# Optimization experiments

Hardware: AMD Instinct MI355X
Metric: run time of the kernel (lower is better)

## Reference

```python
import jax, jax.numpy as jnp
import numpy as np

S, NL = 64, 5000          # num_sequences, num_labels
PD, LD = 1024, 768        # protein / label embedding dims
DIM, OD = 512, 512        # latent_dim, output_dim


def setup_inputs() -> dict:
    key = jax.random.key(0)
    ks = jax.random.split(key, 8)
    sc = lambda f: 1.0 / np.sqrt(f).astype(np.float32)
    return {
        "P_f": jax.random.normal(ks[0], (S, PD), jnp.float32),
        "label_emb": jax.random.normal(ks[1], (NL, LD), jnp.float32),
        "W_p": jax.random.normal(ks[2], (DIM, PD), jnp.float32) * sc(PD),
        "W_l": jax.random.normal(ks[3], (DIM, LD), jnp.float32) * sc(LD),
        "W1": jax.random.normal(ks[4], (OD, 2 * DIM), jnp.float32) * sc(2 * DIM),
        "b1": jnp.zeros((OD,), jnp.float32),
        "W2": jax.random.normal(ks[5], (OD, OD), jnp.float32) * sc(OD),
        "b2": jnp.zeros((OD,), jnp.float32),
        "W3": jax.random.normal(ks[6], (1, OD), jnp.float32) * sc(OD),
        "b3": jnp.zeros((1,), jnp.float32),
        "L": jnp.arange(NL, dtype=jnp.int64),
    }


def reference(P_f, label_emb, W_p, W_l, W1, b1, W2, b2, W3, b3, L):
    # label lookup (cached_label_embeddings(L)) + linear projections
    L_f = label_emb[L]                      # [NL, LD]
    P_e = P_f @ W_p.T                       # [S, DIM]
    L_e = L_f @ W_l.T                       # [NL, DIM]
    # joint cat([P_e_expanded, L_e_expanded]) @ W1.T  ==  P-side + L-side GEMMs,
    # broadcast-summed (avoids materializing the [S*NL, 2*DIM] concat)
    hp = P_e @ W1[:, :DIM].T                # [S, OD]
    hl = L_e @ W1[:, DIM:].T                # [NL, OD]
    h = jax.nn.relu(hp[:, None, :] + hl[None, :, :] + b1)   # [S, NL, OD]
    h = jax.nn.relu(jnp.einsum("snd,od->sno", h, W2) + b2)  # [S, NL, OD]
    logits = jnp.einsum("sno,o->sn", h, W3[0]) + b3[0]      # [S, NL]
    return logits
```

## Files before the change

### kernel.cpp

```cpp
#include <hip/hip_runtime.h>
#include <hip/hip_bf16.h>

typedef short short8 __attribute__((ext_vector_type(8)));
typedef float f32x4 __attribute__((ext_vector_type(4)));

#define S_   64
#define NL_  5000
#define PD_  1024
#define LD_  768
#define DIM_ 512
#define OD_  512

#define BK     32
#define KSTEPS 16
#define NT_M   79
#define HL_RT  157

__device__ __forceinline__ ushort f2bf(float f) {
    union { float f; unsigned u; } v; v.f = f;
    unsigned r = v.u + 0x7fffu + ((v.u >> 16) & 1u);
    return (ushort)(r >> 16);
}
__device__ __forceinline__ float bf2f(ushort h) {
    union { unsigned u; float f; } v; v.u = ((unsigned)h) << 16;
    return v.f;
}
__device__ __forceinline__ int swz(int row, int kslot) {
    return (row * 64 + kslot * 16) ^ (((row >> 1) & 7) << 4);
}

__device__ __forceinline__ void proj8(
    float* Af , const float* __restrict__ A, int lda, int K,
    const float* __restrict__ W, int ldw, const float* __restrict__ bias,
    float* __restrict__ C, int o0, int t) {
    const int s = t & 63, og = t >> 6;
    const int oA = o0 + og * 2, oB = oA + 1;
    float acc0 = 0.f, acc1 = 0.f;
    for (int ck = 0; ck < K; ck += 256) {
        __syncthreads();
#pragma unroll
        for (int it = 0; it < 16; it++) {
            int r = it * 4 + (t >> 6);
            float4 v = *(const float4*)(A + (size_t)r * lda + ck + (t & 63) * 4);
            *(float4*)(Af + r * 258 + (t & 63) * 4) = v;
        }
        __syncthreads();
        const float* w0 = W + (size_t)oA * ldw + ck;
        const float* w1 = W + (size_t)oB * ldw + ck;
        const float* ar = Af + s * 258;
#pragma unroll 8
        for (int k4 = 0; k4 < 64; k4++) {
            f32x4 a4 = *(const f32x4*)(ar + k4 * 4);
            float4 v0 = *(const float4*)(w0 + k4 * 4);
            float4 v1 = *(const float4*)(w1 + k4 * 4);
            acc0 += a4[0] * v0.x + a4[1] * v0.y + a4[2] * v0.z + a4[3] * v0.w;
            acc1 += a4[0] * v1.x + a4[1] * v1.y + a4[2] * v1.z + a4[3] * v1.w;
        }
    }
    C[s * DIM_ + oA] = acc0 + (bias ? bias[oA] : 0.f);
    C[s * DIM_ + oB] = acc1 + (bias ? bias[oB] : 0.f);
}

__global__ __launch_bounds__(256) void k_pre1(
    const float* __restrict__ W2, const float* __restrict__ W_l,
    const float* __restrict__ W1, const float* __restrict__ P_f,
    const float* __restrict__ W_p,
    char* __restrict__ panel, ushort* __restrict__ MlT, float* __restrict__ P_e) {
    __shared__ float lbuf[64 * 258];
    int b = blockIdx.x, t = threadIdx.x;
    if (b < 128) {
        int c = b * 256 + t;
        int o = c >> 6, rem = c & 63, kt = rem >> 2, kslot = rem & 3;
        const float* src = W2 + o * DIM_ + kt * BK + kslot * 8;
        float4 v0 = *(const float4*)src;
        float4 v1 = *(const float4*)(src + 4);
        union { ushort u[8]; short8 v; } pk;
        pk.u[0] = f2bf(v0.x); pk.u[1] = f2bf(v0.y); pk.u[2] = f2bf(v0.z); pk.u[3] = f2bf(v0.w);
        pk.u[4] = f2bf(v1.x); pk.u[5] = f2bf(v1.y); pk.u[6] = f2bf(v1.z); pk.u[7] = f2bf(v1.w);
        *(short8*)(panel + kt * 32768 + (o >> 4) * 1024 + kslot * 256 + (o & 15) * 16) = pk.v;
    } else if (b < 320) {
        float (*w1r)[DIM_] = (float (*)[DIM_])lbuf;
        int bx = b - 128;
        int o0 = (bx / 3) * 8;
        int ld = (bx % 3) * 256 + t;
        for (int i = t; i < 8 * DIM_; i += 256)
            w1r[i >> 9][i & 511] = W1[(o0 + (i >> 9)) * (2 * DIM_) + DIM_ + (i & 511)];
        __syncthreads();
        float acc[8] = {};
        for (int dim = 0; dim < DIM_; dim++) {
            float wl = W_l[dim * LD_ + ld];
#pragma unroll
            for (int oi = 0; oi < 8; oi++) acc[oi] += w1r[oi][dim] * wl;
        }
#pragma unroll
        for (int oi = 0; oi < 8; oi++) MlT[(o0 + oi) * LD_ + ld] = f2bf(acc[oi]);
    } else {
        proj8(lbuf, P_f, PD_, PD_, W_p, PD_, nullptr, P_e, (b - 320) * 8, t);
    }
}

__global__ __launch_bounds__(256) void k_pre2(
    const float* __restrict__ P_e, const float* __restrict__ W1,
    const float* __restrict__ b1, const float* __restrict__ emb,
    const int* __restrict__ L, const ushort* __restrict__ MlT,
    float* __restrict__ hpb, ushort* __restrict__ hlB) {
    __shared__ float lbuf[64 * 258];
    int b = blockIdx.x, t = threadIdx.x;
    if (b < 64) {
        proj8(lbuf, P_e, DIM_, DIM_, W1, 2 * DIM_, b1, hpb, b * 8, t);
    } else {
        int hb = b - 64;
        int rblk = hb % HL_RT, oh = hb / HL_RT;
        int r0 = rblk * 32;
        int w = t >> 6, l = t & 63, lg = l >> 4, ll = l & 15;
        const float* arow[2];
#pragma unroll
        for (int mt = 0; mt < 2; mt++) {
            int r = r0 + mt * 16 + ll;
            if (r >= NL_) r = NL_ - 1;
            arow[mt] = emb + (size_t)L[r] * LD_ + lg * 8;
        }
        f32x4 acc[2][4] = {};
        for (int k = 0; k < LD_; k += 32) {
            short8 a[2], bf[4];
#pragma unroll
            for (int mt = 0; mt < 2; mt++) {
                float4 v0 = *(const float4*)(arow[mt] + k);
                float4 v1 = *(const float4*)(arow[mt] + k + 4);
                union { ushort u[8]; short8 v; } pk;
                pk.u[0] = f2bf(v0.x); pk.u[1] = f2bf(v0.y);
                pk.u[2] = f2bf(v0.z); pk.u[3] = f2bf(v0.w);
                pk.u[4] = f2bf(v1.x); pk.u[5] = f2bf(v1.y);
                pk.u[6] = f2bf(v1.z); pk.u[7] = f2bf(v1.w);
                a[mt] = pk.v;
            }
#pragma unroll
            for (int ot = 0; ot < 4; ot++) {
                int o = oh * 256 + w * 64 + ot * 16 + ll;
                bf[ot] = *(const short8*)(MlT + o * LD_ + k + lg * 8);
            }
#pragma unroll
            for (int mt = 0; mt < 2; mt++)
#pragma unroll
                for (int ot = 0; ot < 4; ot++)
                    acc[mt][ot] = __builtin_amdgcn_mfma_f32_16x16x32_bf16(a[mt], bf[ot], acc[mt][ot], 0, 0, 0);
        }
#pragma unroll
        for (int mt = 0; mt < 2; mt++)
#pragma unroll
            for (int ot = 0; ot < 4; ot++)
#pragma unroll
                for (int reg = 0; reg < 4; reg++) {
                    int r = r0 + mt * 16 + lg * 4 + reg;
                    if (r < NL_)
                        hlB[(size_t)r * DIM_ + oh * 256 + w * 64 + ot * 16 + ll] = f2bf(acc[mt][ot][reg]);
                }
    }
}

__global__ __launch_bounds__(512, 2) void k_main2(
    const ushort* __restrict__ hlB, const float* __restrict__ hpb,
    const char* __restrict__ panel, const float* __restrict__ b2,
    const float* __restrict__ W3, const float* __restrict__ b3,
    float* __restrict__ out) {
    __shared__ f32x4 ldsv[1024];
    char* lds = (char*)ldsv;
    const int t = threadIdx.x;
    const int n0 = blockIdx.x * 64, s0 = blockIdx.y * 2;
    const int w = t >> 6, lane = t & 63, lg = lane >> 4, ll = lane & 15;
    const int wr = w >> 2, wc = w & 3;

    const int arow = t >> 2, akslot = t & 3;
    int an = n0 + (arow & 63); if (an >= NL_) an = NL_ - 1;
    const ushort* hlsrc = hlB + (size_t)an * DIM_ + akslot * 8;
    const float*  hpsrc = hpb + (s0 + (arow >> 6)) * DIM_ + akslot * 8;
    const int awz = swz(arow, akslot);

    const int abase = swz(wr * 64 + ll, lg);
    const char* bbase = panel + (wc * 8) * 1024 + lane * 16;

    f32x4 acc[4][8] = {};

    auto packA = [&](int buf, short8 hv, float4 p0, float4 p1) {
        float hp8[8] = { p0.x, p0.y, p0.z, p0.w, p1.x, p1.y, p1.z, p1.w };
        float x[8];
#pragma unroll
        for (int e = 0; e < 8; e++) {
            float s = bf2f((ushort)hv[e]) + hp8[e];
            x[e] = s > 0.f ? s : 0.f;
        }
        union { __hip_bfloat162 h2[4]; short8 v; } pk;
#pragma unroll
        for (int e = 0; e < 4; e++)
            pk.h2[e] = __float22bfloat162_rn(make_float2(x[2 * e], x[2 * e + 1]));
        *(short8*)(lds + buf * 8192 + awz) = pk.v;
    };

    {
        short8 hv = *(const short8*)(hlsrc);
        float4 p0 = *(const float4*)(hpsrc);
        float4 p1 = *(const float4*)(hpsrc + 4);
        packA(0, hv, p0, p1);
        asm volatile("s_waitcnt lgkmcnt(0)" ::: "memory");
        __builtin_amdgcn_s_barrier();
    }
    short8 bq0[4], bq1[4];
#pragma unroll
    for (int j = 0; j < 4; j++) bq0[j] = *(const short8*)(bbase + j * 1024);

    for (int kt = 0; kt < KSTEPS; kt++) {
        const char* bkt = bbase + kt * 32768;
        short8 hv; float4 p0, p1;
        if (kt + 1 < KSTEPS) {
            hv = *(const short8*)(hlsrc + (kt + 1) * BK);
            p0 = *(const float4*)(hpsrc + (kt + 1) * BK);
            p1 = *(const float4*)(hpsrc + (kt + 1) * BK + 4);
        }
        const char* A = lds + (kt & 1) * 8192;
        short8 a[4];
#pragma unroll
        for (int mt = 0; mt < 4; mt++) a[mt] = *(const short8*)(A + abase + mt * 1024);
#pragma unroll
        for (int j = 0; j < 4; j++) bq1[j] = *(const short8*)(bkt + 4096 + j * 1024);
        __builtin_amdgcn_s_setprio(1);
#pragma unroll
        for (int mt = 0; mt < 4; mt++)
#pragma unroll
            for (int j = 0; j < 4; j++)
                acc[mt][j] = __builtin_amdgcn_mfma_f32_16x16x32_bf16(a[mt], bq0[j], acc[mt][j], 0, 0, 0);
        __builtin_amdgcn_s_setprio(0);
        if (kt + 1 < KSTEPS)
#pragma unroll
            for (int j = 0; j < 4; j++) bq0[j] = *(const short8*)(bkt + 32768 + j * 1024);
        __builtin_amdgcn_s_setprio(1);
#pragma unroll
        for (int mt = 0; mt < 4; mt++)
#pragma unroll
            for (int j = 0; j < 4; j++)
                acc[mt][4 + j] = __builtin_amdgcn_mfma_f32_16x16x32_bf16(a[mt], bq1[j], acc[mt][4 + j], 0, 0, 0);
        __builtin_amdgcn_s_setprio(0);
        if (kt + 1 < KSTEPS) packA((kt + 1) & 1, hv, p0, p1);
        asm volatile("s_waitcnt lgkmcnt(0)" ::: "memory");
        __builtin_amdgcn_s_barrier();
    }

    float* logit = (float*)lds;
    if (t < 128) logit[t] = 0.f;
    __syncthreads();
#pragma unroll
    for (int mt = 0; mt < 4; mt++) {
        float p4[4] = { 0.f, 0.f, 0.f, 0.f };
#pragma unroll
        for (int ot = 0; ot < 8; ot++) {
            int o = wc * 128 + ot * 16 + ll;
            float bb = b2[o], w3 = W3[o];
#pragma unroll
            for (int reg = 0; reg < 4; reg++) {
                float v = acc[mt][ot][reg] + bb;
                v = v > 0.f ? v : 0.f;
                p4[reg] += v * w3;
            }
        }
#pragma unroll
        for (int m = 1; m < 16; m <<= 1)
#pragma unroll
            for (int reg = 0; reg < 4; reg++) p4[reg] += __shfl_xor(p4[reg], m, 64);
        if (ll == 0)
#pragma unroll
            for (int reg = 0; reg < 4; reg++)
                atomicAdd(&logit[wr * 64 + mt * 16 + lg * 4 + reg], p4[reg]);
    }
    __syncthreads();
    if (t < 128) {
        int n = n0 + (t & 63);
        int s = s0 + (t >> 6);
        if (n < NL_) out[(size_t)s * NL_ + n] = logit[t] + b3[0];
    }
}

extern "C" void kernel_launch(void* const* d_in, const int* in_sizes, int n_in,
                              void* d_out, int out_size, void* d_ws, size_t ws_size,
                              hipStream_t stream) {
    const float* P_f = (const float*)d_in[0];
    const float* emb = (const float*)d_in[1];
    const float* W_p = (const float*)d_in[2];
    const float* W_l = (const float*)d_in[3];
    const float* W1  = (const float*)d_in[4];
    const float* b1  = (const float*)d_in[5];
    const float* W2  = (const float*)d_in[6];
    const float* b2  = (const float*)d_in[7];
    const float* W3  = (const float*)d_in[8];
    const float* b3  = (const float*)d_in[9];
    const int*   L   = (const int*)d_in[10];
    float* out = (float*)d_out;

    char* ws = (char*)d_ws;
    size_t off = 0;
    auto alloc = [&](size_t bytes) {
        void* p = ws + off;
        off = (off + bytes + 255) & ~(size_t)255;
        return p;
    };
    char*   panel = (char*)alloc((size_t)KSTEPS * 32768);
    ushort* MlT   = (ushort*)alloc((size_t)OD_ * LD_ * 2);
    float*  P_e   = (float*)alloc((size_t)S_ * DIM_ * 4);
    float*  hpb   = (float*)alloc((size_t)S_ * DIM_ * 4);
    ushort* hlB   = (ushort*)alloc((size_t)NL_ * DIM_ * 2);

    k_pre1<<<384, 256, 0, stream>>>(W2, W_l, W1, P_f, W_p, panel, MlT, P_e);
    k_pre2<<<378, 256, 0, stream>>>(P_e, W1, b1, emb, L, MlT, hpb, hlB);
    k_main2<<<dim3(NT_M, 32), 512, 0, stream>>>(hlB, hpb, panel, b2, W3, b3, out);
}
```

Measured before the change: 273.5 us.

## Give each wave a private A-tile slice to drop per-k-step barriers

Each wave now builds its own copy of the relu(hl+hp) A operand in a private LDS slice, with each lane handling one row. This removes the block-wide barrier after every k-step. The cost is redundant global loads and conversion work, since the four waves sharing a row group each rebuild the same tile. LDS use also grows fourfold to 64KB, which may reduce occupancy below 2 blocks per CU, and the loads within a step are no longer prefetched one iteration ahead.

```diff
diff --git a/kernel.cpp b/kernel.cpp
--- a/kernel.cpp
+++ b/kernel.cpp
@@ -24,9 +24,6 @@
 __device__ __forceinline__ float bf2f(ushort h) {
     union { unsigned u; float f; } v; v.u = ((unsigned)h) << 16;
     return v.f;
-}
-__device__ __forceinline__ int swz(int row, int kslot) {
-    return (row * 64 + kslot * 16) ^ (((row >> 1) & 7) << 4);
 }
 
 __device__ __forceinline__ void proj8(
@@ -163,63 +160,57 @@
     const char* __restrict__ panel, const float* __restrict__ b2,
     const float* __restrict__ W3, const float* __restrict__ b3,
     float* __restrict__ out) {
-    __shared__ f32x4 ldsv[1024];
+    __shared__ f32x4 ldsv[4096];
     char* lds = (char*)ldsv;
     const int t = threadIdx.x;
     const int n0 = blockIdx.x * 64, s0 = blockIdx.y * 2;
     const int w = t >> 6, lane = t & 63, lg = lane >> 4, ll = lane & 15;
     const int wr = w >> 2, wc = w & 3;
 
-    const int arow = t >> 2, akslot = t & 3;
-    int an = n0 + (arow & 63); if (an >= NL_) an = NL_ - 1;
-    const ushort* hlsrc = hlB + (size_t)an * DIM_ + akslot * 8;
-    const float*  hpsrc = hpb + (s0 + (arow >> 6)) * DIM_ + akslot * 8;
-    const int awz = swz(arow, akslot);
-
-    const int abase = swz(wr * 64 + ll, lg);
+    int an = n0 + lane; if (an >= NL_) an = NL_ - 1;
+    const ushort* hlsrc = hlB + (size_t)an * DIM_;
+    const float*  hpsrc = hpb + (s0 + wr) * DIM_;
+    char* slice = lds + w * 8192;
+    const int rdbase = lg * 1024 + ll * 16;
+
     const char* bbase = panel + (wc * 8) * 1024 + lane * 16;
 
     f32x4 acc[4][8] = {};
 
-    auto packA = [&](int buf, short8 hv, float4 p0, float4 p1) {
-        float hp8[8] = { p0.x, p0.y, p0.z, p0.w, p1.x, p1.y, p1.z, p1.w };
-        float x[8];
-#pragma unroll
-        for (int e = 0; e < 8; e++) {
-            float s = bf2f((ushort)hv[e]) + hp8[e];
-            x[e] = s > 0.f ? s : 0.f;
-        }
-        union { __hip_bfloat162 h2[4]; short8 v; } pk;
-#pragma unroll
-        for (int e = 0; e < 4; e++)
-            pk.h2[e] = __float22bfloat162_rn(make_float2(x[2 * e], x[2 * e + 1]));
-        *(short8*)(lds + buf * 8192 + awz) = pk.v;
+    auto packA = [&](int kt, int buf) {
+        char* dst = slice + buf * 4096;
+#pragma unroll
+        for (int c = 0; c < 4; c++) {
+            short8 hv = *(const short8*)(hlsrc + kt * BK + c * 8);
+            f32x4 p0 = *(const f32x4*)(hpsrc + kt * BK + c * 8);
+            f32x4 p1 = *(const f32x4*)(hpsrc + kt * BK + c * 8 + 4);
+            float x[8];
+#pragma unroll
+            for (int e = 0; e < 4; e++) {
+                float s0f = bf2f((ushort)hv[e]) + p0[e];
+                float s1f = bf2f((ushort)hv[4 + e]) + p1[e];
+                x[e]     = s0f > 0.f ? s0f : 0.f;
+                x[4 + e] = s1f > 0.f ? s1f : 0.f;
+            }
+            union { __hip_bfloat162 h2[4]; short8 v; } pk;
+#pragma unroll
+            for (int e = 0; e < 4; e++)
+                pk.h2[e] = __float22bfloat162_rn(make_float2(x[2 * e], x[2 * e + 1]));
+            *(short8*)(dst + c * 1024 + lane * 16) = pk.v;
+        }
     };
 
-    {
-        short8 hv = *(const short8*)(hlsrc);
-        float4 p0 = *(const float4*)(hpsrc);
-        float4 p1 = *(const float4*)(hpsrc + 4);
-        packA(0, hv, p0, p1);
-        asm volatile("s_waitcnt lgkmcnt(0)" ::: "memory");
-        __builtin_amdgcn_s_barrier();
-    }
+    packA(0, 0);
     short8 bq0[4], bq1[4];
 #pragma unroll
     for (int j = 0; j < 4; j++) bq0[j] = *(const short8*)(bbase + j * 1024);
 
     for (int kt = 0; kt < KSTEPS; kt++) {
         const char* bkt = bbase + kt * 32768;
-        short8 hv; float4 p0, p1;
-        if (kt + 1 < KSTEPS) {
-            hv = *(const short8*)(hlsrc + (kt + 1) * BK);
-            p0 = *(const float4*)(hpsrc + (kt + 1) * BK);
-            p1 = *(const float4*)(hpsrc + (kt + 1) * BK + 4);
-        }
-        const char* A = lds + (kt & 1) * 8192;
+        const char* A = slice + (kt & 1) * 4096;
         short8 a[4];
 #pragma unroll
-        for (int mt = 0; mt < 4; mt++) a[mt] = *(const short8*)(A + abase + mt * 1024);
+        for (int mt = 0; mt < 4; mt++) a[mt] = *(const short8*)(A + rdbase + mt * 256);
 #pragma unroll
         for (int j = 0; j < 4; j++) bq1[j] = *(const short8*)(bkt + 4096 + j * 1024);
         __builtin_amdgcn_s_setprio(1);
@@ -239,11 +230,10 @@
             for (int j = 0; j < 4; j++)
                 acc[mt][4 + j] = __builtin_amdgcn_mfma_f32_16x16x32_bf16(a[mt], bq1[j], acc[mt][4 + j], 0, 0, 0);
         __builtin_amdgcn_s_setprio(0);
-        if (kt + 1 < KSTEPS) packA((kt + 1) & 1, hv, p0, p1);
-        asm volatile("s_waitcnt lgkmcnt(0)" ::: "memory");
-        __builtin_amdgcn_s_barrier();
-    }
-
+        if (kt + 1 < KSTEPS) packA(kt + 1, (kt + 1) & 1);
+    }
+
+    __syncthreads();
     float* logit = (float*)lds;
     if (t < 128) logit[t] = 0.f;
     __syncthreads();
```

New measurement: 411.2 us. 1.5x slower.

## Widen A-tile LDS staging to 4-kstep windows and unroll W_l projection loop

Applied to the files above, without the earlier changes.

The main kernel now stages four K-steps of the relu'd A operand per LDS buffer, double-buffered as 2x32KB. It synchronises once per window instead of once per K-step and interleaves global loads and packing of the next window with the MFMA work. This is meant to cut barrier count and hide the latency of the hl/hp loads. The cost is LDS growing from 16KB to 64KB per block, which may limit occupancy against the launch_bounds(512,2) target. The W_l·W1 precompute loop is also unrolled by 4 with vectorised LDS reads of W1 rows.

```diff
diff --git a/kernel.cpp b/kernel.cpp
--- a/kernel.cpp
+++ b/kernel.cpp
@@ -12,6 +12,7 @@
 #define OD_  512
 
 #define BK     32
+#define NWIN4  4
 #define KSTEPS 16
 #define NT_M   79
 #define HL_RT  157
@@ -87,10 +88,16 @@
             w1r[i >> 9][i & 511] = W1[(o0 + (i >> 9)) * (2 * DIM_) + DIM_ + (i & 511)];
         __syncthreads();
         float acc[8] = {};
-        for (int dim = 0; dim < DIM_; dim++) {
-            float wl = W_l[dim * LD_ + ld];
-#pragma unroll
-            for (int oi = 0; oi < 8; oi++) acc[oi] += w1r[oi][dim] * wl;
+        for (int dim = 0; dim < DIM_; dim += 4) {
+            float wl0 = W_l[(dim + 0) * LD_ + ld];
+            float wl1 = W_l[(dim + 1) * LD_ + ld];
+            float wl2 = W_l[(dim + 2) * LD_ + ld];
+            float wl3 = W_l[(dim + 3) * LD_ + ld];
+#pragma unroll
+            for (int oi = 0; oi < 8; oi++) {
+                f32x4 wv = *(const f32x4*)&w1r[oi][dim];
+                acc[oi] += wv[0] * wl0 + wv[1] * wl1 + wv[2] * wl2 + wv[3] * wl3;
+            }
         }
 #pragma unroll
         for (int oi = 0; oi < 8; oi++) MlT[(o0 + oi) * LD_ + ld] = f2bf(acc[oi]);
@@ -163,7 +170,7 @@
     const char* __restrict__ panel, const float* __restrict__ b2,
     const float* __restrict__ W3, const float* __restrict__ b3,
     float* __restrict__ out) {
-    __shared__ f32x4 ldsv[1024];
+    __shared__ f32x4 ldsv[4096];
     char* lds = (char*)ldsv;
     const int t = threadIdx.x;
     const int n0 = blockIdx.x * 64, s0 = blockIdx.y * 2;
@@ -181,26 +188,30 @@
 
     f32x4 acc[4][8] = {};
 
-    auto packA = [&](int buf, short8 hv, float4 p0, float4 p1) {
-        float hp8[8] = { p0.x, p0.y, p0.z, p0.w, p1.x, p1.y, p1.z, p1.w };
+    auto packSub = [&](int buf, int sub, short8 hv, f32x4 p0, f32x4 p1) {
         float x[8];
 #pragma unroll
-        for (int e = 0; e < 8; e++) {
-            float s = bf2f((ushort)hv[e]) + hp8[e];
-            x[e] = s > 0.f ? s : 0.f;
+        for (int e = 0; e < 4; e++) {
+            float a0 = bf2f((ushort)hv[e]) + p0[e];
+            float a1 = bf2f((ushort)hv[4 + e]) + p1[e];
+            x[e]     = a0 > 0.f ? a0 : 0.f;
+            x[4 + e] = a1 > 0.f ? a1 : 0.f;
         }
         union { __hip_bfloat162 h2[4]; short8 v; } pk;
 #pragma unroll
         for (int e = 0; e < 4; e++)
             pk.h2[e] = __float22bfloat162_rn(make_float2(x[2 * e], x[2 * e + 1]));
-        *(short8*)(lds + buf * 8192 + awz) = pk.v;
+        *(short8*)(lds + buf * 32768 + sub * 8192 + awz) = pk.v;
     };
 
     {
-        short8 hv = *(const short8*)(hlsrc);
-        float4 p0 = *(const float4*)(hpsrc);
-        float4 p1 = *(const float4*)(hpsrc + 4);
-        packA(0, hv, p0, p1);
+#pragma unroll
+        for (int i = 0; i < 4; i++) {
+            short8 hv = *(const short8*)(hlsrc + i * BK);
+            f32x4 p0 = *(const f32x4*)(hpsrc + i * BK);
+            f32x4 p1 = *(const f32x4*)(hpsrc + i * BK + 4);
+            packSub(0, i, hv, p0, p1);
+        }
         asm volatile("s_waitcnt lgkmcnt(0)" ::: "memory");
         __builtin_amdgcn_s_barrier();
     }
@@ -208,38 +219,64 @@
 #pragma unroll
     for (int j = 0; j < 4; j++) bq0[j] = *(const short8*)(bbase + j * 1024);
 
-    for (int kt = 0; kt < KSTEPS; kt++) {
-        const char* bkt = bbase + kt * 32768;
-        short8 hv; float4 p0, p1;
-        if (kt + 1 < KSTEPS) {
-            hv = *(const short8*)(hlsrc + (kt + 1) * BK);
-            p0 = *(const float4*)(hpsrc + (kt + 1) * BK);
-            p1 = *(const float4*)(hpsrc + (kt + 1) * BK + 4);
-        }
-        const char* A = lds + (kt & 1) * 8192;
-        short8 a[4];
-#pragma unroll
-        for (int mt = 0; mt < 4; mt++) a[mt] = *(const short8*)(A + abase + mt * 1024);
-#pragma unroll
-        for (int j = 0; j < 4; j++) bq1[j] = *(const short8*)(bkt + 4096 + j * 1024);
-        __builtin_amdgcn_s_setprio(1);
-#pragma unroll
-        for (int mt = 0; mt < 4; mt++)
-#pragma unroll
-            for (int j = 0; j < 4; j++)
-                acc[mt][j] = __builtin_amdgcn_mfma_f32_16x16x32_bf16(a[mt], bq0[j], acc[mt][j], 0, 0, 0);
-        __builtin_amdgcn_s_setprio(0);
-        if (kt + 1 < KSTEPS)
-#pragma unroll
-            for (int j = 0; j < 4; j++) bq0[j] = *(const short8*)(bkt + 32768 + j * 1024);
-        __builtin_amdgcn_s_setprio(1);
-#pragma unroll
-        for (int mt = 0; mt < 4; mt++)
-#pragma unroll
-            for (int j = 0; j < 4; j++)
-                acc[mt][4 + j] = __builtin_amdgcn_mfma_f32_16x16x32_bf16(a[mt], bq1[j], acc[mt][4 + j], 0, 0, 0);
-        __builtin_amdgcn_s_setprio(0);
-        if (kt + 1 < KSTEPS) packA((kt + 1) & 1, hv, p0, p1);
+    short8 hvA, hvB; f32x4 pA0, pA1, pB0, pB1;
+
+    for (int win = 0; win < NWIN4; win++) {
+        const char* A = lds + (win & 1) * 32768;
+        const int nxt = (win & 1) ^ 1;
+        const bool more = (win + 1 < NWIN4);
+#pragma unroll
+        for (int i = 0; i < 4; i++) {
+            const int ks = 4 * win + i;
+            const char* bks = bbase + ks * 32768;
+            short8 a[4];
+#pragma unroll
+            for (int mt = 0; mt < 4; mt++)
+                a[mt] = *(const short8*)(A + i * 8192 + abase + mt * 1024);
+#pragma unroll
+            for (int j = 0; j < 4; j++) bq1[j] = *(const short8*)(bks + 4096 + j * 1024);
+            if (more) {
+                if (i == 0) {
+                    hvA = *(const short8*)(hlsrc + (ks + 4) * BK);
+                    pA0 = *(const f32x4*)(hpsrc + (ks + 4) * BK);
+                    pA1 = *(const f32x4*)(hpsrc + (ks + 4) * BK + 4);
+                } else if (i == 1) {
+                    packSub(nxt, 0, hvA, pA0, pA1);
+                    hvB = *(const short8*)(hlsrc + (ks + 4) * BK);
+                    pB0 = *(const f32x4*)(hpsrc + (ks + 4) * BK);
+                    pB1 = *(const f32x4*)(hpsrc + (ks + 4) * BK + 4);
+                } else if (i == 2) {
+                    packSub(nxt, 1, hvB, pB0, pB1);
+                    hvA = *(const short8*)(hlsrc + (ks + 4) * BK);
+                    pA0 = *(const f32x4*)(hpsrc + (ks + 4) * BK);
+                    pA1 = *(const f32x4*)(hpsrc + (ks + 4) * BK + 4);
+                } else {
+                    packSub(nxt, 2, hvA, pA0, pA1);
+                    hvB = *(const short8*)(hlsrc + (ks + 4) * BK);
+                    pB0 = *(const f32x4*)(hpsrc + (ks + 4) * BK);
+                    pB1 = *(const f32x4*)(hpsrc + (ks + 4) * BK + 4);
+                }
+            }
+            __builtin_amdgcn_s_setprio(1);
+#pragma unroll
+            for (int mt = 0; mt < 4; mt++)
+#pragma unroll
+                for (int j = 0; j < 4; j++)
+                    acc[mt][j] = __builtin_amdgcn_mfma_f32_16x16x32_bf16(a[mt], bq0[j], acc[mt][j], 0, 0, 0);
+            __builtin_amdgcn_s_setprio(0);
+            if (!(win == NWIN4 - 1 && i == 3))
+#pragma unroll
+                for (int j = 0; j < 4; j++)
+                    bq0[j] = *(const short8*)(bbase + (ks + 1) * 32768 + j * 1024);
+            __builtin_amdgcn_s_setprio(1);
+#pragma unroll
+            for (int mt = 0; mt < 4; mt++)
+#pragma unroll
+                for (int j = 0; j < 4; j++)
+                    acc[mt][4 + j] = __builtin_amdgcn_mfma_f32_16x16x32_bf16(a[mt], bq1[j], acc[mt][4 + j], 0, 0, 0);
+            __builtin_amdgcn_s_setprio(0);
+        }
+        if (more) packSub(nxt, 3, hvB, pB0, pB1);
         asm volatile("s_waitcnt lgkmcnt(0)" ::: "memory");
         __builtin_amdgcn_s_barrier();
     }
```

New measurement: 241.5 us. 1.13x faster.
